# Performance work log

Measured on AMD Instinct MI355X. Metric: run time of the kernel, lower is better.

Reference implementation:

```python
import jax, jax.numpy as jnp
import numpy as np

EPS_BN = 1e-3   # nn.BatchNorm1d(eps=0.001)
LAMDA = 1e-5    # Point_Attentation.lamda


def _bn(x, g, b, m, v):
    # inference-mode BatchNorm1d over last dim
    return (x - m) * (g * jax.lax.rsqrt(v + EPS_BN)) + b


def _forward(features_low, features_high,
             bott_W, bott_b, bott_gamma, bott_beta, bott_mean, bott_var,
             qkv_W, qkv_gamma, qkv_beta, qkv_mean, qkv_var,
             mlp_W, mlp_gamma, mlp_beta, mlp_mean, mlp_var,
             fus_W, fus_b, fus_gamma, fus_beta, fus_mean, fus_var,
             batch_size):
    N, C = features_low.shape
    B = batch_size
    n = N // B  # points per batch segment (equal-length segments)

    # ---- Point_Attentation: per-point channel mean, var over channels / (n-1) ----
    x = features_low
    mean = jnp.mean(x, axis=-1, keepdims=True)
    d = x - mean
    var = jnp.sum(d * d, axis=-1, keepdims=True) / (n - 1)
    e_t = d * d / (4.0 * (var + LAMDA)) + 0.5
    x = x + jax.nn.sigmoid(e_t) * x

    for i in range(3):
        y = jax.nn.relu(_bn(x @ bott_W[2 * i] + bott_b[2 * i],
                            bott_gamma[2 * i], bott_beta[2 * i], bott_mean[2 * i], bott_var[2 * i]))
        y = jax.nn.relu(_bn(y @ bott_W[2 * i + 1] + bott_b[2 * i + 1],
                            bott_gamma[2 * i + 1], bott_beta[2 * i + 1], bott_mean[2 * i + 1], bott_var[2 * i + 1]))
        x = x + y

    # ---- fusion: per-batch QKV attention between low (x) and high features ----
    low = x.reshape(B, n, C)
    high = features_high.reshape(B, n, C)

    q = _bn(jnp.einsum('bnc,cd->bnd', low, qkv_W[0]), qkv_gamma[0], qkv_beta[0], qkv_mean[0], qkv_var[0])
    k = _bn(jnp.einsum('bnc,cd->bnd', high, qkv_W[1]), qkv_gamma[1], qkv_beta[1], qkv_mean[1], qkv_var[1])
    v = _bn(jnp.einsum('bnc,cd->bnd', high, qkv_W[2]), qkv_gamma[2], qkv_beta[2], qkv_mean[2], qkv_var[2])

    scale = 1.0 / jnp.sqrt(jnp.asarray(256.0, dtype=q.dtype))  # normal_dim = 256
    attn = jax.nn.softmax(jnp.einsum('bqc,bkc->bqk', q, k) * scale, axis=-1)
    ao = jnp.einsum('bqk,bkc->bqc', attn, v)

    # mlp: (Linear no-bias -> BN -> Dropout(eval=id) -> ReLU) x2
    h = jax.nn.relu(_bn(jnp.einsum('bnc,cd->bnd', ao, mlp_W[0]), mlp_gamma[0], mlp_beta[0], mlp_mean[0], mlp_var[0]))
    h = jax.nn.relu(_bn(jnp.einsum('bnc,cd->bnd', h, mlp_W[1]), mlp_gamma[1], mlp_beta[1], mlp_mean[1], mlp_var[1]))

    # linear_fusion: Linear(2C->C, bias) -> BN -> ReLU
    cat = jnp.concatenate([low, h], axis=-1)  # [B, n, 2C]
    out = jax.nn.relu(_bn(jnp.einsum('bnc,cd->bnd', cat, fus_W) + fus_b, fus_gamma, fus_beta, fus_mean, fus_var))
    return out.reshape(N, C)


def setup_inputs() -> dict:
    key = jax.random.key(0)
    ks = jax.random.split(key, 16)
    N, C, B = 16384, 256, 4
    s = 0.05
    d = {}
    d['features_low'] = jax.random.normal(ks[0], (N, C), jnp.float32)
    d['features_high'] = jax.random.normal(ks[1], (N, C), jnp.float32)
    d['bott_W'] = jax.random.normal(ks[2], (6, C, C), jnp.float32) * s
    d['bott_b'] = jnp.zeros((6, C), jnp.float32)
    d['bott_gamma'] = jnp.ones((6, C), jnp.float32)
    d['bott_beta'] = jnp.zeros((6, C), jnp.float32)
    d['bott_mean'] = jnp.zeros((6, C), jnp.float32)
    d['bott_var'] = jnp.ones((6, C), jnp.float32)
    d['qkv_W'] = jax.random.normal(ks[3], (3, C, C), jnp.float32) * s
    d['qkv_gamma'] = jnp.ones((3, C), jnp.float32)
    d['qkv_beta'] = jnp.zeros((3, C), jnp.float32)
    d['qkv_mean'] = jnp.zeros((3, C), jnp.float32)
    d['qkv_var'] = jnp.ones((3, C), jnp.float32)
    d['mlp_W'] = jax.random.normal(ks[4], (2, C, C), jnp.float32) * s
    d['mlp_gamma'] = jnp.ones((2, C), jnp.float32)
    d['mlp_beta'] = jnp.zeros((2, C), jnp.float32)
    d['mlp_mean'] = jnp.zeros((2, C), jnp.float32)
    d['mlp_var'] = jnp.ones((2, C), jnp.float32)
    d['fus_W'] = jax.random.normal(ks[5], (2 * C, C), jnp.float32) * s
    d['fus_b'] = jnp.zeros((C,), jnp.float32)
    d['fus_gamma'] = jnp.ones((C,), jnp.float32)
    d['fus_beta'] = jnp.zeros((C,), jnp.float32)
    d['fus_mean'] = jnp.zeros((C,), jnp.float32)
    d['fus_var'] = jnp.ones((C,), jnp.float32)
    d['batch_size'] = B
    return d


def reference(features_low, features_high,
              bott_W, bott_b, bott_gamma, bott_beta, bott_mean, bott_var,
              qkv_W, qkv_gamma, qkv_beta, qkv_mean, qkv_var,
              mlp_W, mlp_gamma, mlp_beta, mlp_mean, mlp_var,
              fus_W, fus_b, fus_gamma, fus_beta, fus_mean, fus_var,
              batch_size):
    return _forward(features_low, features_high,
                    bott_W, bott_b, bott_gamma, bott_beta, bott_mean, bott_var,
                    qkv_W, qkv_gamma, qkv_beta, qkv_mean, qkv_var,
                    mlp_W, mlp_gamma, mlp_beta, mlp_mean, mlp_var,
                    fus_W, fus_b, fus_gamma, fus_beta, fus_mean, fus_var,
                    batch_size)
```

## Files before the change

kernel.cpp:

```cpp
#include <hip/hip_runtime.h>
#include <cstdint>
#include <cstddef>

typedef float v4f __attribute__((ext_vector_type(4)));
typedef float v2f __attribute__((ext_vector_type(2)));
typedef short v8s __attribute__((ext_vector_type(8)));
typedef unsigned short v4u __attribute__((ext_vector_type(4)));

typedef unsigned short ubf;

#define NPTS 16384
#define CD   256
#define NBAT 4
#define NPB  4096

__device__ __forceinline__ float bf2f(ubf u) {
    union { unsigned u; float f; } c; c.u = ((unsigned)u) << 16; return c.f;
}
__device__ __forceinline__ ubf f2bf(float f) {
    union { float f; unsigned u; } c; c.f = f;
    unsigned u = c.u;
    u += 0x7fffu + ((u >> 16) & 1u);
    return (ubf)(u >> 16);
}

__global__ __launch_bounds__(256) void k_pre(
    const float* __restrict__ low, float* __restrict__ xout,
    const float* __restrict__ bott, const float* __restrict__ qkv,
    const float* __restrict__ mlp, const float* __restrict__ fus,
    ubf* __restrict__ wt) {
    const int bid = blockIdx.x;
    if (bid < 4096) {
        const int lane = threadIdx.x & 63;
        const int row  = bid * 4 + (threadIdx.x >> 6);
        const float* p = low + (size_t)row * CD + lane * 4;
        v4f v = *reinterpret_cast<const v4f*>(p);
        float d[4];
        float s = v[0] + v[1] + v[2] + v[3];
#pragma unroll
        for (int o = 32; o >= 1; o >>= 1) s += __shfl_xor(s, o);
        const float mean = s * (1.0f / 256.0f);
        float ss = 0.f;
#pragma unroll
        for (int i = 0; i < 4; ++i) { d[i] = v[i] - mean; ss += d[i] * d[i]; }
#pragma unroll
        for (int o = 32; o >= 1; o >>= 1) ss += __shfl_xor(ss, o);
        const float var = ss * (1.0f / 4095.0f);
        const float dn  = 1.0f / (4.0f * (var + 1e-5f));
        v4f o;
#pragma unroll
        for (int i = 0; i < 4; ++i) {
            const float e   = d[i] * d[i] * dn + 0.5f;
            const float sig = 1.0f / (1.0f + __expf(-e));
            o[i] = v[i] * (1.0f + sig);
        }
        *reinterpret_cast<v4f*>(xout + (size_t)row * CD + lane * 4) = o;
        return;
    }
    const int bid2 = bid - 4096;
    const int z = bid2 >> 7, r = bid2 & 127;
    const float* src; int K; size_t doff;
    if (z < 6)       { src = bott + (size_t)z * 65536;       K = 256; doff = (size_t)z * 65536; }
    else if (z < 9)  { src = qkv  + (size_t)(z - 6) * 65536; K = 256; doff = (size_t)z * 65536; }
    else if (z < 11) { src = mlp  + (size_t)(z - 9) * 65536; K = 256; doff = (size_t)z * 65536; }
    else             { src = fus;                            K = 512; doff = (size_t)11 * 65536; }
    const int kt = (r >> 3) * 32, nt = (r & 7) * 32;
    if (kt >= K) return;
    __shared__ ubf tile[32][33];
    const int tx = threadIdx.x & 31, ty = threadIdx.x >> 5;
#pragma unroll
    for (int i = 0; i < 4; ++i)
        tile[ty * 4 + i][tx] = f2bf(src[(size_t)(kt + ty * 4 + i) * 256 + nt + tx]);
    __syncthreads();
    ubf* dst = wt + doff;
#pragma unroll
    for (int i = 0; i < 4; ++i)
        dst[(size_t)(nt + ty * 4 + i) * K + kt + tx] = tile[tx][ty * 4 + i];
}

__global__ __launch_bounds__(256) void k_conv1(
    float* __restrict__ xA, const ubf* __restrict__ wT,
    const float* __restrict__ bb, const float* __restrict__ bg,
    const float* __restrict__ bbe, const float* __restrict__ bm_,
    const float* __restrict__ bv) {
    __shared__ __attribute__((aligned(16))) float xls[64 * 256];
    __shared__ __attribute__((aligned(16))) ubf   yls[64 * 256];

    const int lane = threadIdx.x & 63;
    const int w    = threadIdx.x >> 6;
    const int wr = w >> 1, wc = w & 1;
    const int q15 = lane & 15, g = lane >> 4;
    const int bm = blockIdx.x * 64;

    {
        float* xsrcb = xA + (size_t)bm * 256;
#pragma unroll
        for (int it = 0; it < 16; ++it) {
            const int L4 = (it * 256 + w * 64) * 4;
            const int Ll = L4 + lane * 4;
            const int row = Ll >> 8, col = (Ll & 255) ^ ((row & 7) << 3);
            __builtin_amdgcn_global_load_lds(
                (const __attribute__((address_space(1))) unsigned*)(xsrcb + row * 256 + col),
                (__attribute__((address_space(3))) unsigned*)(xls + L4), 16, 0, 0);
        }
    }
    __syncthreads();

    const int r0l = wr * 32 + q15;
#pragma unroll 1
    for (int s = 0; s < 3; ++s) {
        const ubf* W0 = wT + (size_t)(2 * s) * 65536;
        const ubf* W1 = wT + (size_t)(2 * s + 1) * 65536;

        v4f acc[2][8];
#pragma unroll
        for (int i = 0; i < 2; ++i)
#pragma unroll
            for (int j = 0; j < 8; ++j)
#pragma unroll
                for (int r = 0; r < 4; ++r) acc[i][j][r] = 0.f;
        for (int ks = 0; ks < 8; ++ks) {
            const int k0 = ks * 32 + g * 8;
            v8s afr[2], bfr[8];
#pragma unroll
            for (int mi = 0; mi < 2; ++mi) {
                const int row = r0l + mi * 16;
                const float* ap = &xls[row * 256 + (k0 ^ ((row & 7) << 3))];
                v4f a = *reinterpret_cast<const v4f*>(ap);
                v4f b = *reinterpret_cast<const v4f*>(ap + 4);
                v8s t;
#pragma unroll
                for (int j = 0; j < 4; ++j) { t[j] = (short)f2bf(a[j]); t[j + 4] = (short)f2bf(b[j]); }
                afr[mi] = t;
            }
#pragma unroll
            for (int ni = 0; ni < 8; ++ni)
                bfr[ni] = *reinterpret_cast<const v8s*>(W0 + (size_t)(wc * 128 + ni * 16 + q15) * 256 + k0);
#pragma unroll
            for (int mi = 0; mi < 2; ++mi)
#pragma unroll
                for (int ni = 0; ni < 8; ++ni)
                    acc[mi][ni] = __builtin_amdgcn_mfma_f32_16x16x32_bf16(afr[mi], bfr[ni], acc[mi][ni], 0, 0, 0);
        }
#pragma unroll
        for (int ni = 0; ni < 8; ++ni) {
            const int col = wc * 128 + ni * 16 + q15;
            const float sc  = bg[2 * s * 256 + col] * rsqrtf(bv[2 * s * 256 + col] + 1e-3f);
            const float tc  = bbe[2 * s * 256 + col] - bm_[2 * s * 256 + col] * sc;
            const float bia = bb[2 * s * 256 + col];
#pragma unroll
            for (int mi = 0; mi < 2; ++mi)
#pragma unroll
                for (int r = 0; r < 4; ++r) {
                    const int row = wr * 32 + mi * 16 + g * 4 + r;
                    float z = (acc[mi][ni][r] + bia) * sc + tc;
                    z = fmaxf(z, 0.f);
                    yls[row * 256 + (col ^ ((row & 7) << 3))] = f2bf(z);
                }
        }
        __syncthreads();

#pragma unroll
        for (int i = 0; i < 2; ++i)
#pragma unroll
            for (int j = 0; j < 8; ++j)
#pragma unroll
                for (int r = 0; r < 4; ++r) acc[i][j][r] = 0.f;
        for (int ks = 0; ks < 8; ++ks) {
            const int k0 = ks * 32 + g * 8;
            v8s afr[2], bfr[8];
#pragma unroll
            for (int mi = 0; mi < 2; ++mi) {
                const int row = r0l + mi * 16;
                afr[mi] = *reinterpret_cast<const v8s*>(&yls[row * 256 + (k0 ^ ((row & 7) << 3))]);
            }
#pragma unroll
            for (int ni = 0; ni < 8; ++ni)
                bfr[ni] = *reinterpret_cast<const v8s*>(W1 + (size_t)(wc * 128 + ni * 16 + q15) * 256 + k0);
#pragma unroll
            for (int mi = 0; mi < 2; ++mi)
#pragma unroll
                for (int ni = 0; ni < 8; ++ni)
                    acc[mi][ni] = __builtin_amdgcn_mfma_f32_16x16x32_bf16(afr[mi], bfr[ni], acc[mi][ni], 0, 0, 0);
        }
#pragma unroll
        for (int ni = 0; ni < 8; ++ni) {
            const int col = wc * 128 + ni * 16 + q15;
            const int c1 = (2 * s + 1) * 256 + col;
            const float sc  = bg[c1] * rsqrtf(bv[c1] + 1e-3f);
            const float tc  = bbe[c1] - bm_[c1] * sc;
            const float bia = bb[c1];
#pragma unroll
            for (int mi = 0; mi < 2; ++mi)
#pragma unroll
                for (int r = 0; r < 4; ++r) {
                    const int row = wr * 32 + mi * 16 + g * 4 + r;
                    float z = (acc[mi][ni][r] + bia) * sc + tc;
                    z = fmaxf(z, 0.f);
                    xls[row * 256 + (col ^ ((row & 7) << 3))] += z;
                }
        }
        __syncthreads();
    }

    {
        float* xdstb = xA + (size_t)bm * 256;
#pragma unroll
        for (int it = 0; it < 16; ++it) {
            const int Ll = (it * 256 + threadIdx.x) * 4;
            const int row = Ll >> 8, cl = Ll & 255;
            const int gcol = cl ^ ((row & 7) << 3);
            *reinterpret_cast<v4f*>(xdstb + row * 256 + gcol) =
                *reinterpret_cast<const v4f*>(xls + Ll);
        }
    }
}

__global__ __launch_bounds__(256) void k_qkv(
    const float* __restrict__ xA, const float* __restrict__ fh,
    const ubf* __restrict__ wTq,
    const float* __restrict__ qg, const float* __restrict__ qbe,
    const float* __restrict__ qm, const float* __restrict__ qv,
    ubf* __restrict__ qB, ubf* __restrict__ kB, ubf* __restrict__ vT) {
    const int m = blockIdx.y >> 1;
    const float* Af = (m == 0) ? xA : fh;
    const ubf* WT = wTq + m * 65536;
    const float* gamma = qg + m * 256;
    const float* beta  = qbe + m * 256;
    const float* bmean = qm + m * 256;
    const float* bvar  = qv + m * 256;

    const int lane = threadIdx.x & 63;
    const int w    = threadIdx.x >> 6;
    const int wr = w >> 1, wc = w & 1;
    const int q15 = lane & 15, g = lane >> 4;
    const int bm = blockIdx.x * 128, bn = (blockIdx.y & 1) * 128;
    const int r0 = bm + wr * 64 + q15;
    const int c0 = bn + wc * 64 + q15;

    v4f acc[4][4];
#pragma unroll
    for (int i = 0; i < 4; ++i)
#pragma unroll
        for (int j = 0; j < 4; ++j)
#pragma unroll
            for (int r = 0; r < 4; ++r) acc[i][j][r] = 0.f;

    for (int ks = 0; ks < 8; ++ks) {
        const int k0 = ks * 32 + g * 8;
        v8s afr[4], bfr[4];
#pragma unroll
        for (int mi = 0; mi < 4; ++mi) {
            const float* ap = Af + (size_t)(r0 + mi * 16) * CD + k0;
            v4f a = *reinterpret_cast<const v4f*>(ap);
            v4f b = *reinterpret_cast<const v4f*>(ap + 4);
            v8s t;
#pragma unroll
            for (int j = 0; j < 4; ++j) { t[j] = (short)f2bf(a[j]); t[j + 4] = (short)f2bf(b[j]); }
            afr[mi] = t;
        }
#pragma unroll
        for (int ni = 0; ni < 4; ++ni)
            bfr[ni] = *reinterpret_cast<const v8s*>(WT + (size_t)(c0 + ni * 16) * 256 + k0);
#pragma unroll
        for (int mi = 0; mi < 4; ++mi)
#pragma unroll
            for (int ni = 0; ni < 4; ++ni)
                acc[mi][ni] = __builtin_amdgcn_mfma_f32_16x16x32_bf16(afr[mi], bfr[ni], acc[mi][ni], 0, 0, 0);
    }

    ubf* outb = (m == 0) ? qB : kB;
#pragma unroll
    for (int ni = 0; ni < 4; ++ni) {
        const int col = c0 + ni * 16;
        const float sc = gamma[col] * rsqrtf(bvar[col] + 1e-3f);
        const float tc = beta[col] - bmean[col] * sc;
#pragma unroll
        for (int mi = 0; mi < 4; ++mi) {
            if (m == 2) {
                const int row0 = bm + wr * 64 + mi * 16 + g * 4;
                v4u pk;
#pragma unroll
                for (int r = 0; r < 4; ++r) pk[r] = f2bf(acc[mi][ni][r] * sc + tc);
                const int bb = row0 >> 12, key = row0 & 4095;
                *reinterpret_cast<v4u*>(vT + ((size_t)(bb * CD + col)) * NPB + key) = pk;
            } else {
#pragma unroll
                for (int r = 0; r < 4; ++r) {
                    const int row = bm + wr * 64 + mi * 16 + g * 4 + r;
                    outb[(size_t)row * CD + col] = f2bf(acc[mi][ni][r] * sc + tc);
                }
            }
        }
    }
}

__device__ __forceinline__ void stage_k256(const ubf* __restrict__ kg,
                                           ubf* kd, int wave, int lane) {
#pragma unroll
    for (int it = 0; it < 8; ++it) {
        const int Lb = it * 2048 + wave * 512;
        const int L  = Lb + lane * 8;
        const int key = L >> 8, c8 = (L & 255) ^ ((key & 7) << 3);
        __builtin_amdgcn_global_load_lds(
            (const __attribute__((address_space(1))) unsigned*)(kg + key * CD + c8),
            (__attribute__((address_space(3))) unsigned*)(kd + Lb), 16, 0, 0);
    }
}
__device__ __forceinline__ void stage_v256(const ubf* __restrict__ vg,
                                           ubf* vd, int wave, int lane) {
#pragma unroll
    for (int it = 0; it < 8; ++it) {
        const int Lb = it * 2048 + wave * 512;
        const int L  = Lb + lane * 8;
        const int c = L >> 6, k8 = (L & 63) ^ ((c & 7) << 3);
        __builtin_amdgcn_global_load_lds(
            (const __attribute__((address_space(1))) unsigned*)(vg + (size_t)c * NPB + k8),
            (__attribute__((address_space(3))) unsigned*)(vd + Lb), 16, 0, 0);
    }
}

__global__ __launch_bounds__(256) void k_attn(const ubf* __restrict__ qb, const ubf* __restrict__ kb,
                                              const ubf* __restrict__ vt,
                                              ubf* __restrict__ o0, ubf* __restrict__ o1,
                                              float* __restrict__ ml) {
    __shared__ __attribute__((aligned(16))) ubf kls[64 * 256];
    __shared__ __attribute__((aligned(16))) ubf vls[256 * 64];
    __shared__ __attribute__((aligned(16))) ubf pls[4 * 16 * 64];

    const int raw = blockIdx.x;
    const int xcd = raw & 7, qt = raw >> 3;
    const int b = xcd >> 1, half = xcd & 1;

    const int wave = threadIdx.x >> 6, lane = threadIdx.x & 63;
    const int q15 = lane & 15, g = lane >> 4;

    const ubf* qrow = qb + ((size_t)(b * NPB + qt * 64 + wave * 16 + q15)) * CD + g * 8;
    v8s qf[8];
#pragma unroll
    for (int cs = 0; cs < 8; ++cs) qf[cs] = *reinterpret_cast<const v8s*>(qrow + cs * 32);

    v4f oacc[16];
#pragma unroll
    for (int i = 0; i < 16; ++i)
#pragma unroll
        for (int r = 0; r < 4; ++r) oacc[i][r] = 0.f;
    float m_run = -3.0e38f, l_run = 0.f;

    const ubf* kgb = kb + ((size_t)(b * NPB) + half * 2048) * CD;
    const ubf* vgb = vt + (size_t)b * CD * NPB + half * 2048;
    ubf* pw = pls + wave * 1024;

    stage_k256(kgb, kls, wave, lane);
    __syncthreads();

    for (int kc = 0; kc < 32; ++kc) {
        stage_v256(vgb + kc * 64, vls, wave, lane);

        v4f sacc[4];
#pragma unroll
        for (int f = 0; f < 4; ++f)
#pragma unroll
            for (int r = 0; r < 4; ++r) sacc[f][r] = 0.f;
#pragma unroll
        for (int cs = 0; cs < 8; ++cs)
#pragma unroll
            for (int f = 0; f < 4; ++f) {
                const int key = 16 * f + q15;
                v8s af = *reinterpret_cast<const v8s*>(&kls[(key * CD + cs * 32 + g * 8) ^ ((key & 7) << 3)]);
                sacc[f] = __builtin_amdgcn_mfma_f32_16x16x32_bf16(af, qf[cs], sacc[f], 0, 0, 0);
            }

        __syncthreads();
        if (kc + 1 < 32)
            stage_k256(kgb + (size_t)(kc + 1) * 64 * CD, kls, wave, lane);

        float mloc = -3.0e38f;
#pragma unroll
        for (int f = 0; f < 4; ++f)
#pragma unroll
            for (int r = 0; r < 4; ++r) {
                float x = sacc[f][r] * 0.0625f;
                sacc[f][r] = x;
                mloc = fmaxf(mloc, x);
            }
        mloc = fmaxf(mloc, __shfl_xor(mloc, 16));
        mloc = fmaxf(mloc, __shfl_xor(mloc, 32));
        if (!__all(mloc <= m_run + 8.0f)) {
            const float mnew  = fmaxf(m_run, mloc);
            const float alpha = __expf(m_run - mnew);
            l_run *= alpha;
#pragma unroll
            for (int i = 0; i < 16; ++i)
#pragma unroll
                for (int r = 0; r < 4; ++r) oacc[i][r] *= alpha;
            m_run = mnew;
        }
        float lloc = 0.f;
#pragma unroll
        for (int f = 0; f < 4; ++f)
#pragma unroll
            for (int r = 0; r < 4; ++r) {
                float p = __expf(sacc[f][r] - m_run);
                sacc[f][r] = p;
                lloc += p;
            }
        lloc += __shfl_xor(lloc, 16);
        lloc += __shfl_xor(lloc, 32);
        l_run += lloc;

#pragma unroll
        for (int f = 0; f < 4; ++f) {
            unsigned u0, u1, u2, u3;
            { union { float f; unsigned u; } c; c.f = sacc[f][0]; u0 = c.u; }
            { union { float f; unsigned u; } c; c.f = sacc[f][1]; u1 = c.u; }
            { union { float f; unsigned u; } c; c.f = sacc[f][2]; u2 = c.u; }
            { union { float f; unsigned u; } c; c.f = sacc[f][3]; u3 = c.u; }
            unsigned p01 = (u0 >> 16) | (u1 & 0xFFFF0000u);
            unsigned p23 = (u2 >> 16) | (u3 & 0xFFFF0000u);
            const int e = q15 * 64 + 16 * f + 4 * g;
            *reinterpret_cast<unsigned*>(&pw[(e)     ^ ((q15 & 7) << 3)]) = p01;
            *reinterpret_cast<unsigned*>(&pw[(e + 2) ^ ((q15 & 7) << 3)]) = p23;
        }
        v8s pb0 = *reinterpret_cast<const v8s*>(&pw[(q15 * 64 +  0 + 8 * g) ^ ((q15 & 7) << 3)]);
        v8s pb1 = *reinterpret_cast<const v8s*>(&pw[(q15 * 64 + 32 + 8 * g) ^ ((q15 & 7) << 3)]);
#pragma unroll
        for (int mt = 0; mt < 16; ++mt) {
            const int c = 16 * mt + q15;
            v8s av0 = *reinterpret_cast<const v8s*>(&vls[(c * 64 +  0 + 8 * g) ^ ((c & 7) << 3)]);
            oacc[mt] = __builtin_amdgcn_mfma_f32_16x16x32_bf16(av0, pb0, oacc[mt], 0, 0, 0);
            v8s av1 = *reinterpret_cast<const v8s*>(&vls[(c * 64 + 32 + 8 * g) ^ ((c & 7) << 3)]);
            oacc[mt] = __builtin_amdgcn_mfma_f32_16x16x32_bf16(av1, pb1, oacc[mt], 0, 0, 0);
        }

        __syncthreads();
    }

    const int grow = b * NPB + qt * 64 + wave * 16 + q15;
    ubf* aor = (half ? o1 : o0) + (size_t)grow * CD;
#pragma unroll
    for (int mt = 0; mt < 16; ++mt) {
        v4u pk;
#pragma unroll
        for (int r = 0; r < 4; ++r) pk[r] = f2bf(oacc[mt][r]);
        *reinterpret_cast<v4u*>(aor + 16 * mt + 4 * g) = pk;
    }
    if (g == 0) {
        v2f d; d[0] = m_run; d[1] = l_run;
        *reinterpret_cast<v2f*>(ml + (size_t)(half * NPTS + grow) * 2) = d;
    }
}

__global__ __launch_bounds__(256) void k_tail(
    const ubf* __restrict__ o0, const ubf* __restrict__ o1, const float* __restrict__ ml,
    const float* __restrict__ xA, const ubf* __restrict__ wT,
    const float* __restrict__ mg, const float* __restrict__ mbe,
    const float* __restrict__ mm, const float* __restrict__ mv,
    const float* __restrict__ fb, const float* __restrict__ fg,
    const float* __restrict__ fbe, const float* __restrict__ fm,
    const float* __restrict__ fv, float* __restrict__ out) {
    __shared__ __attribute__((aligned(16))) ubf yls[64 * 256];

    const int lane = threadIdx.x & 63;
    const int w    = threadIdx.x >> 6;
    const int wr = w >> 1, wc = w & 1;
    const int q15 = lane & 15, g = lane >> 4;
    const int bm = blockIdx.x * 64;
    const int r0l = wr * 32 + q15;

    const ubf* W9  = wT + (size_t)9 * 65536;
    const ubf* W10 = wT + (size_t)10 * 65536;
    const ubf* W11 = wT + (size_t)11 * 65536;

    v4f acc[2][8];

    float a0[2], a1[2];
#pragma unroll
    for (int mi = 0; mi < 2; ++mi) {
        const int row = bm + r0l + mi * 16;
        const float m0 = ml[2 * row],          l0 = ml[2 * row + 1];
        const float m1 = ml[2 * (NPTS + row)], l1 = ml[2 * (NPTS + row) + 1];
        const float mx = fmaxf(m0, m1);
        const float w0 = __expf(m0 - mx), w1 = __expf(m1 - mx);
        const float inv = 1.0f / (w0 * l0 + w1 * l1);
        a0[mi] = w0 * inv; a1[mi] = w1 * inv;
    }
#pragma unroll
    for (int i = 0; i < 2; ++i)
#pragma unroll
        for (int j = 0; j < 8; ++j)
#pragma unroll
            for (int r = 0; r < 4; ++r) acc[i][j][r] = 0.f;
    for (int ks = 0; ks < 8; ++ks) {
        const int k0 = ks * 32 + g * 8;
        v8s afr[2], bfr[8];
#pragma unroll
        for (int mi = 0; mi < 2; ++mi) {
            const int row = bm + r0l + mi * 16;
            v8s u0 = *reinterpret_cast<const v8s*>(o0 + (size_t)row * CD + k0);
            v8s u1 = *reinterpret_cast<const v8s*>(o1 + (size_t)row * CD + k0);
            v8s t;
#pragma unroll
            for (int j = 0; j < 8; ++j)
                t[j] = (short)f2bf(a0[mi] * bf2f((ubf)u0[j]) + a1[mi] * bf2f((ubf)u1[j]));
            afr[mi] = t;
        }
#pragma unroll
        for (int ni = 0; ni < 8; ++ni)
            bfr[ni] = *reinterpret_cast<const v8s*>(W9 + (size_t)(wc * 128 + ni * 16 + q15) * 256 + k0);
#pragma unroll
        for (int mi = 0; mi < 2; ++mi)
#pragma unroll
            for (int ni = 0; ni < 8; ++ni)
                acc[mi][ni] = __builtin_amdgcn_mfma_f32_16x16x32_bf16(afr[mi], bfr[ni], acc[mi][ni], 0, 0, 0);
    }
#pragma unroll
    for (int ni = 0; ni < 8; ++ni) {
        const int col = wc * 128 + ni * 16 + q15;
        const float sc = mg[col] * rsqrtf(mv[col] + 1e-3f);
        const float tc = mbe[col] - mm[col] * sc;
#pragma unroll
        for (int mi = 0; mi < 2; ++mi)
#pragma unroll
            for (int r = 0; r < 4; ++r) {
                const int row = wr * 32 + mi * 16 + g * 4 + r;
                float z = fmaxf(acc[mi][ni][r] * sc + tc, 0.f);
                yls[row * 256 + (col ^ ((row & 7) << 3))] = f2bf(z);
            }
    }
    __syncthreads();

#pragma unroll
    for (int i = 0; i < 2; ++i)
#pragma unroll
        for (int j = 0; j < 8; ++j)
#pragma unroll
            for (int r = 0; r < 4; ++r) acc[i][j][r] = 0.f;
    for (int ks = 0; ks < 8; ++ks) {
        const int k0 = ks * 32 + g * 8;
        v8s afr[2], bfr[8];
#pragma unroll
        for (int mi = 0; mi < 2; ++mi) {
            const int row = r0l + mi * 16;
            afr[mi] = *reinterpret_cast<const v8s*>(&yls[row * 256 + (k0 ^ ((row & 7) << 3))]);
        }
#pragma unroll
        for (int ni = 0; ni < 8; ++ni)
            bfr[ni] = *reinterpret_cast<const v8s*>(W10 + (size_t)(wc * 128 + ni * 16 + q15) * 256 + k0);
#pragma unroll
        for (int mi = 0; mi < 2; ++mi)
#pragma unroll
            for (int ni = 0; ni < 8; ++ni)
                acc[mi][ni] = __builtin_amdgcn_mfma_f32_16x16x32_bf16(afr[mi], bfr[ni], acc[mi][ni], 0, 0, 0);
    }
    __syncthreads();
#pragma unroll
    for (int ni = 0; ni < 8; ++ni) {
        const int col = wc * 128 + ni * 16 + q15;
        const float sc = mg[256 + col] * rsqrtf(mv[256 + col] + 1e-3f);
        const float tc = mbe[256 + col] - mm[256 + col] * sc;
#pragma unroll
        for (int mi = 0; mi < 2; ++mi)
#pragma unroll
            for (int r = 0; r < 4; ++r) {
                const int row = wr * 32 + mi * 16 + g * 4 + r;
                float z = fmaxf(acc[mi][ni][r] * sc + tc, 0.f);
                yls[row * 256 + (col ^ ((row & 7) << 3))] = f2bf(z);
            }
    }
    __syncthreads();

#pragma unroll
    for (int i = 0; i < 2; ++i)
#pragma unroll
        for (int j = 0; j < 8; ++j)
#pragma unroll
            for (int r = 0; r < 4; ++r) acc[i][j][r] = 0.f;
    for (int ks = 0; ks < 16; ++ks) {
        const int k0 = ks * 32 + g * 8;
        v8s afr[2], bfr[8];
#pragma unroll
        for (int mi = 0; mi < 2; ++mi) {
            if (k0 < 256) {
                const float* ap = xA + (size_t)(bm + r0l + mi * 16) * CD + k0;
                v4f a = *reinterpret_cast<const v4f*>(ap);
                v4f b = *reinterpret_cast<const v4f*>(ap + 4);
                v8s t;
#pragma unroll
                for (int j = 0; j < 4; ++j) { t[j] = (short)f2bf(a[j]); t[j + 4] = (short)f2bf(b[j]); }
                afr[mi] = t;
            } else {
                const int row = r0l + mi * 16, kk = k0 - 256;
                afr[mi] = *reinterpret_cast<const v8s*>(&yls[row * 256 + (kk ^ ((row & 7) << 3))]);
            }
        }
#pragma unroll
        for (int ni = 0; ni < 8; ++ni)
            bfr[ni] = *reinterpret_cast<const v8s*>(W11 + (size_t)(wc * 128 + ni * 16 + q15) * 512 + k0);
#pragma unroll
        for (int mi = 0; mi < 2; ++mi)
#pragma unroll
            for (int ni = 0; ni < 8; ++ni)
                acc[mi][ni] = __builtin_amdgcn_mfma_f32_16x16x32_bf16(afr[mi], bfr[ni], acc[mi][ni], 0, 0, 0);
    }
#pragma unroll
    for (int ni = 0; ni < 8; ++ni) {
        const int col = wc * 128 + ni * 16 + q15;
        const float sc = fg[col] * rsqrtf(fv[col] + 1e-3f);
        const float tc = fbe[col] - fm[col] * sc;
        const float bia = fb[col];
#pragma unroll
        for (int mi = 0; mi < 2; ++mi)
#pragma unroll
            for (int r = 0; r < 4; ++r) {
                const int row = bm + wr * 32 + mi * 16 + g * 4 + r;
                float z = fmaxf((acc[mi][ni][r] + bia) * sc + tc, 0.f);
                out[(size_t)row * CD + col] = z;
            }
    }
}

extern "C" void kernel_launch(void* const* d_in, const int* in_sizes, int n_in,
                              void* d_out, int out_size, void* d_ws, size_t ws_size,
                              hipStream_t stream) {
    const float* f_low   = (const float*)d_in[0];
    const float* f_high  = (const float*)d_in[1];
    const float* bott_W  = (const float*)d_in[2];
    const float* bott_b  = (const float*)d_in[3];
    const float* bott_g  = (const float*)d_in[4];
    const float* bott_be = (const float*)d_in[5];
    const float* bott_m  = (const float*)d_in[6];
    const float* bott_v  = (const float*)d_in[7];
    const float* qkv_W   = (const float*)d_in[8];
    const float* qkv_g   = (const float*)d_in[9];
    const float* qkv_be  = (const float*)d_in[10];
    const float* qkv_m   = (const float*)d_in[11];
    const float* qkv_v   = (const float*)d_in[12];
    const float* mlp_W   = (const float*)d_in[13];
    const float* mlp_g   = (const float*)d_in[14];
    const float* mlp_be  = (const float*)d_in[15];
    const float* mlp_m   = (const float*)d_in[16];
    const float* mlp_v   = (const float*)d_in[17];
    const float* fus_W   = (const float*)d_in[18];
    const float* fus_b   = (const float*)d_in[19];
    const float* fus_g   = (const float*)d_in[20];
    const float* fus_be  = (const float*)d_in[21];
    const float* fus_m   = (const float*)d_in[22];
    const float* fus_v   = (const float*)d_in[23];
    (void)in_sizes; (void)n_in; (void)out_size; (void)ws_size;

    char* ws = (char*)d_ws;
    const size_t MB = 1024 * 1024;
    float* xA = (float*)(ws);
    ubf*   o0 = (ubf*)  (ws + 17 * MB);
    ubf*   qB = (ubf*)  (ws + 26 * MB);
    ubf*   kB = (ubf*)  (ws + 35 * MB);
    ubf*   vT = (ubf*)  (ws + 44 * MB);
    ubf*   wT = (ubf*)  (ws + 53 * MB);
    ubf*   o1 = (ubf*)  (ws + 56 * MB);
    float* ml = (float*)(ws + 65 * MB);

    k_pre<<<dim3(4096 + 1536), dim3(256), 0, stream>>>(f_low, xA,
                                                       bott_W, qkv_W, mlp_W, fus_W, wT);

    k_conv1<<<dim3(256), dim3(256), 0, stream>>>(xA, wT,
                                                 bott_b, bott_g, bott_be, bott_m, bott_v);

    k_qkv<<<dim3(128, 6), dim3(256), 0, stream>>>(xA, f_high, wT + (size_t)6 * 65536,
                                                  qkv_g, qkv_be, qkv_m, qkv_v, qB, kB, vT);

    k_attn<<<dim3(512), dim3(256), 0, stream>>>(qB, kB, vT, o0, o1, ml);

    k_tail<<<dim3(256), dim3(256), 0, stream>>>(o0, o1, ml, xA, wT,
                                                mlp_g, mlp_be, mlp_m, mlp_v,
                                                fus_b, fus_g, fus_be, fus_m, fus_v,
                                                (float*)d_out);
}
```

Before: 305.3 us.

## Shrink attention tiles to 32 queries and 32-key chunks with 128-thread blocks

The flash-attention kernel now uses 2 waves per block (32 query rows) and 32-key chunks instead of 4 waves and 64-key chunks, doubling the grid to 1024 blocks. V for the next chunk is staged after the second barrier instead of at the start of the iteration, and V is laid out in LDS as column pairs. The smaller LDS footprint and launch bounds are meant to raise occupancy and grid parallelism. The cost is twice the loop iterations and barriers per key span, and each K/V chunk is reused by fewer queries, so global and L2 traffic increases. The fmaxf edits in conv1 are cosmetic.

```diff
diff --git a/kernel.cpp b/kernel.cpp
--- a/kernel.cpp
+++ b/kernel.cpp
@@ -153,8 +153,7 @@
 #pragma unroll
                 for (int r = 0; r < 4; ++r) {
                     const int row = wr * 32 + mi * 16 + g * 4 + r;
-                    float z = (acc[mi][ni][r] + bia) * sc + tc;
-                    z = fmaxf(z, 0.f);
+                    float z = fmaxf((acc[mi][ni][r] + bia) * sc + tc, 0.f);
                     yls[row * 256 + (col ^ ((row & 7) << 3))] = f2bf(z);
                 }
         }
@@ -195,8 +194,7 @@
 #pragma unroll
                 for (int r = 0; r < 4; ++r) {
                     const int row = wr * 32 + mi * 16 + g * 4 + r;
-                    float z = (acc[mi][ni][r] + bia) * sc + tc;
-                    z = fmaxf(z, 0.f);
+                    float z = fmaxf((acc[mi][ni][r] + bia) * sc + tc, 0.f);
                     xls[row * 256 + (col ^ ((row & 7) << 3))] += z;
                 }
         }
@@ -295,11 +293,11 @@
     }
 }
 
-__device__ __forceinline__ void stage_k256(const ubf* __restrict__ kg,
-                                           ubf* kd, int wave, int lane) {
+__device__ __forceinline__ void stage_k32(const ubf* __restrict__ kg,
+                                          ubf* kd, int wave, int lane) {
 #pragma unroll
     for (int it = 0; it < 8; ++it) {
-        const int Lb = it * 2048 + wave * 512;
+        const int Lb = it * 1024 + wave * 512;
         const int L  = Lb + lane * 8;
         const int key = L >> 8, c8 = (L & 255) ^ ((key & 7) << 3);
         __builtin_amdgcn_global_load_lds(
@@ -307,26 +305,28 @@
             (__attribute__((address_space(3))) unsigned*)(kd + Lb), 16, 0, 0);
     }
 }
-__device__ __forceinline__ void stage_v256(const ubf* __restrict__ vg,
-                                           ubf* vd, int wave, int lane) {
+__device__ __forceinline__ void stage_v32(const ubf* __restrict__ vg,
+                                          ubf* vd, int wave, int lane) {
 #pragma unroll
     for (int it = 0; it < 8; ++it) {
-        const int Lb = it * 2048 + wave * 512;
+        const int Lb = it * 1024 + wave * 512;
         const int L  = Lb + lane * 8;
-        const int c = L >> 6, k8 = (L & 63) ^ ((c & 7) << 3);
+        const int cpair = L >> 6;
+        const int rem   = (L & 63) ^ ((cpair & 7) << 3);
+        const int c = cpair * 2 + (rem >> 5), k = rem & 31;
         __builtin_amdgcn_global_load_lds(
-            (const __attribute__((address_space(1))) unsigned*)(vg + (size_t)c * NPB + k8),
+            (const __attribute__((address_space(1))) unsigned*)(vg + (size_t)c * NPB + k),
             (__attribute__((address_space(3))) unsigned*)(vd + Lb), 16, 0, 0);
     }
 }
 
-__global__ __launch_bounds__(256) void k_attn(const ubf* __restrict__ qb, const ubf* __restrict__ kb,
-                                              const ubf* __restrict__ vt,
-                                              ubf* __restrict__ o0, ubf* __restrict__ o1,
-                                              float* __restrict__ ml) {
-    __shared__ __attribute__((aligned(16))) ubf kls[64 * 256];
-    __shared__ __attribute__((aligned(16))) ubf vls[256 * 64];
-    __shared__ __attribute__((aligned(16))) ubf pls[4 * 16 * 64];
+__global__ __launch_bounds__(128, 2) void k_attn(const ubf* __restrict__ qb, const ubf* __restrict__ kb,
+                                                 const ubf* __restrict__ vt,
+                                                 ubf* __restrict__ o0, ubf* __restrict__ o1,
+                                                 float* __restrict__ ml) {
+    __shared__ __attribute__((aligned(16))) ubf kls[32 * 256];
+    __shared__ __attribute__((aligned(16))) ubf vls[128 * 64];
+    __shared__ __attribute__((aligned(16))) ubf pls[2 * 1024];
 
     const int raw = blockIdx.x;
     const int xcd = raw & 7, qt = raw >> 3;
@@ -334,8 +334,9 @@
 
     const int wave = threadIdx.x >> 6, lane = threadIdx.x & 63;
     const int q15 = lane & 15, g = lane >> 4;
-
-    const ubf* qrow = qb + ((size_t)(b * NPB + qt * 64 + wave * 16 + q15)) * CD + g * 8;
+    const int swzP = (q15 & 7) << 3;
+
+    const ubf* qrow = qb + ((size_t)(b * NPB + qt * 32 + wave * 16 + q15)) * CD + g * 8;
     v8s qf[8];
 #pragma unroll
     for (int cs = 0; cs < 8; ++cs) qf[cs] = *reinterpret_cast<const v8s*>(qrow + cs * 32);
@@ -351,33 +352,32 @@
     const ubf* vgb = vt + (size_t)b * CD * NPB + half * 2048;
     ubf* pw = pls + wave * 1024;
 
-    stage_k256(kgb, kls, wave, lane);
+    stage_k32(kgb, kls, wave, lane);
+    stage_v32(vgb, vls, wave, lane);
     __syncthreads();
 
-    for (int kc = 0; kc < 32; ++kc) {
-        stage_v256(vgb + kc * 64, vls, wave, lane);
-
-        v4f sacc[4];
-#pragma unroll
-        for (int f = 0; f < 4; ++f)
+    for (int kc = 0; kc < 64; ++kc) {
+        v4f sacc[2];
+#pragma unroll
+        for (int f = 0; f < 2; ++f)
 #pragma unroll
             for (int r = 0; r < 4; ++r) sacc[f][r] = 0.f;
 #pragma unroll
         for (int cs = 0; cs < 8; ++cs)
 #pragma unroll
-            for (int f = 0; f < 4; ++f) {
+            for (int f = 0; f < 2; ++f) {
                 const int key = 16 * f + q15;
                 v8s af = *reinterpret_cast<const v8s*>(&kls[(key * CD + cs * 32 + g * 8) ^ ((key & 7) << 3)]);
                 sacc[f] = __builtin_amdgcn_mfma_f32_16x16x32_bf16(af, qf[cs], sacc[f], 0, 0, 0);
             }
 
         __syncthreads();
-        if (kc + 1 < 32)
-            stage_k256(kgb + (size_t)(kc + 1) * 64 * CD, kls, wave, lane);
+        if (kc + 1 < 64)
+            stage_k32(kgb + (size_t)(kc + 1) * 32 * CD, kls, wave, lane);
 
         float mloc = -3.0e38f;
 #pragma unroll
-        for (int f = 0; f < 4; ++f)
+        for (int f = 0; f < 2; ++f)
 #pragma unroll
             for (int r = 0; r < 4; ++r) {
                 float x = sacc[f][r] * 0.0625f;
@@ -398,7 +398,7 @@
         }
         float lloc = 0.f;
 #pragma unroll
-        for (int f = 0; f < 4; ++f)
+        for (int f = 0; f < 2; ++f)
 #pragma unroll
             for (int r = 0; r < 4; ++r) {
                 float p = __expf(sacc[f][r] - m_run);
@@ -410,7 +410,7 @@
         l_run += lloc;
 
 #pragma unroll
-        for (int f = 0; f < 4; ++f) {
+        for (int f = 0; f < 2; ++f) {
             unsigned u0, u1, u2, u3;
             { union { float f; unsigned u; } c; c.f = sacc[f][0]; u0 = c.u; }
             { union { float f; unsigned u; } c; c.f = sacc[f][1]; u1 = c.u; }
@@ -419,24 +419,24 @@
             unsigned p01 = (u0 >> 16) | (u1 & 0xFFFF0000u);
             unsigned p23 = (u2 >> 16) | (u3 & 0xFFFF0000u);
             const int e = q15 * 64 + 16 * f + 4 * g;
-            *reinterpret_cast<unsigned*>(&pw[(e)     ^ ((q15 & 7) << 3)]) = p01;
-            *reinterpret_cast<unsigned*>(&pw[(e + 2) ^ ((q15 & 7) << 3)]) = p23;
-        }
-        v8s pb0 = *reinterpret_cast<const v8s*>(&pw[(q15 * 64 +  0 + 8 * g) ^ ((q15 & 7) << 3)]);
-        v8s pb1 = *reinterpret_cast<const v8s*>(&pw[(q15 * 64 + 32 + 8 * g) ^ ((q15 & 7) << 3)]);
+            *reinterpret_cast<unsigned*>(&pw[(e)     ^ swzP]) = p01;
+            *reinterpret_cast<unsigned*>(&pw[(e + 2) ^ swzP]) = p23;
+        }
+        v8s pb = *reinterpret_cast<const v8s*>(&pw[(q15 * 64 + 8 * g) ^ swzP]);
 #pragma unroll
         for (int mt = 0; mt < 16; ++mt) {
-            const int c = 16 * mt + q15;
-            v8s av0 = *reinterpret_cast<const v8s*>(&vls[(c * 64 +  0 + 8 * g) ^ ((c & 7) << 3)]);
-            oacc[mt] = __builtin_amdgcn_mfma_f32_16x16x32_bf16(av0, pb0, oacc[mt], 0, 0, 0);
-            v8s av1 = *reinterpret_cast<const v8s*>(&vls[(c * 64 + 32 + 8 * g) ^ ((c & 7) << 3)]);
-            oacc[mt] = __builtin_amdgcn_mfma_f32_16x16x32_bf16(av1, pb1, oacc[mt], 0, 0, 0);
+            const int cp = 8 * mt + (q15 >> 1);
+            const int e  = cp * 64 + ((((q15 & 1) << 5) | (g << 3)) ^ ((q15 >> 1) << 3));
+            v8s av = *reinterpret_cast<const v8s*>(&vls[e]);
+            oacc[mt] = __builtin_amdgcn_mfma_f32_16x16x32_bf16(av, pb, oacc[mt], 0, 0, 0);
         }
 
         __syncthreads();
-    }
-
-    const int grow = b * NPB + qt * 64 + wave * 16 + q15;
+        if (kc + 1 < 64)
+            stage_v32(vgb + (kc + 1) * 32, vls, wave, lane);
+    }
+
+    const int grow = b * NPB + qt * 32 + wave * 16 + q15;
     ubf* aor = (half ? o1 : o0) + (size_t)grow * CD;
 #pragma unroll
     for (int mt = 0; mt < 16; ++mt) {
@@ -669,7 +669,7 @@
     k_qkv<<<dim3(128, 6), dim3(256), 0, stream>>>(xA, f_high, wT + (size_t)6 * 65536,
                                                   qkv_g, qkv_be, qkv_m, qkv_v, qB, kB, vT);
 
-    k_attn<<<dim3(512), dim3(256), 0, stream>>>(qB, kB, vT, o0, o1, ml);
+    k_attn<<<dim3(1024), dim3(128), 0, stream>>>(qB, kB, vT, o0, o1, ml);
 
     k_tail<<<dim3(256), dim3(256), 0, stream>>>(o0, o1, ml, xA, wT,
                                                 mlp_g, mlp_be, mlp_m, mlp_v,
```

New measurement: 305.5 us. About the same (+0.1%).
